# Optimization experiments

Measured on AMD Instinct MI355X. Metric: run time of the kernel, lower is better.

## Reference

```python
import jax, jax.numpy as jnp
import numpy as np

BITS = 8
EPS = 1e-08
D_IN = 4096
D_OUT = 4096


def setup_inputs() -> dict:
    key = jax.random.key(0)
    k1, k2, k3 = jax.random.split(key, 3)
    hidden_states = jax.random.normal(k1, (4, 2048, D_IN), dtype=jnp.float32)
    # Pre-quantized (dequantized-value) weight buffer, as the module stores it in float
    qmax = 2 ** (BITS - 1) - 1
    w = jax.random.normal(k2, (D_IN, D_OUT), dtype=jnp.float32) * 0.02
    w_scale = jnp.max(jnp.abs(w)) / qmax
    weight_quantized = jnp.clip(jnp.round(w / w_scale), -qmax, qmax) * w_scale
    bias = jax.random.normal(k3, (D_OUT,), dtype=jnp.float32) * 0.01
    x_scale = jnp.asarray(3.0, dtype=jnp.float32)  # calibrated activation maxabs
    return {
        "hidden_states": hidden_states,
        "weight_quantized": weight_quantized,
        "x_scale": x_scale,
        "bias": bias,
    }


def _quantize_maxabs(x, scale, bits, eps):
    # scalar max-abs quantization with a fixed (calibrated) scale
    qmax = 2 ** (bits - 1) - 1
    step = jnp.maximum(scale, eps) / qmax
    return jnp.clip(jnp.round(x / step), -qmax, qmax) * step


def reference(hidden_states, weight_quantized, x_scale, bias):
    orig_shape = hidden_states.shape[:-1]
    d = hidden_states.shape[-1]
    x_flat = hidden_states.reshape(-1, d)
    x_q = _quantize_maxabs(x_flat, x_scale, BITS, EPS).astype(weight_quantized.dtype)
    out = x_q @ weight_quantized  # [tokens, d_out]
    out = out + bias.astype(out.dtype)[None, :]
    out = out.astype(hidden_states.dtype)
    return out.reshape(*orig_shape, weight_quantized.shape[1])
```

## Files before the change

kernel.cpp:

```cpp
#include <hip/hip_runtime.h>
#include <hip/hip_bf16.h>
#include <cstdint>

#define D_IN  4096
#define D_OUT 4096

typedef __attribute__((ext_vector_type(4)))  int   i32x4;

typedef const __attribute__((address_space(1))) unsigned g_u32;
typedef __attribute__((address_space(3))) unsigned       l_u32;

__global__ void prep_kernel(const float* __restrict__ W, int nw,
                            const float* __restrict__ x,
                            char* __restrict__ xq,
                            const float* __restrict__ xscale, int nx,
                            unsigned* __restrict__ wsp) {
    int tid = threadIdx.x;
    if (blockIdx.x < 1024) {
        __shared__ float red[256];
        float m = 0.f;
        for (int i = (blockIdx.x * 256 + tid) * 4; i < nw; i += 1024 * 256 * 4) {
            float4 v = *(const float4*)(W + i);
            m = fmaxf(m, fmaxf(fmaxf(fabsf(v.x), fabsf(v.y)),
                               fmaxf(fabsf(v.z), fabsf(v.w))));
        }
        red[tid] = m; __syncthreads();
        for (int s = 128; s > 0; s >>= 1) {
            if (tid < s) red[tid] = fmaxf(red[tid], red[tid + s]);
            __syncthreads();
        }
        if (tid == 0) atomicMax(wsp, __float_as_uint(red[0]));
    } else {
        int i = ((blockIdx.x - 1024) * 256 + tid) * 4;
        if (i >= nx) return;
        float inv = 127.0f / fmaxf(xscale[0], 1e-8f);
        float4 v = *(const float4*)(x + i);
        char4 o;
        o.x = (char)fminf(fmaxf(rintf(v.x * inv), -127.f), 127.f);
        o.y = (char)fminf(fmaxf(rintf(v.y * inv), -127.f), 127.f);
        o.z = (char)fminf(fmaxf(rintf(v.z * inv), -127.f), 127.f);
        o.w = (char)fminf(fmaxf(rintf(v.w * inv), -127.f), 127.f);
        *(char4*)(xq + i) = o;
    }
}

__global__ void convW_kernel(const float* __restrict__ W,
                             char* __restrict__ Wt,
                             const unsigned* __restrict__ wsp) {
    __shared__ float tile[64][65];
    const float wmax = __uint_as_float(wsp[0]);
    const float inv  = 127.0f / wmax;
    const int n0 = blockIdx.x * 64, k0 = blockIdx.y * 64;
    const int t = threadIdx.x;
    {
        const int r = t >> 2, c0 = (t & 3) * 16;
        const float* src = W + (size_t)(k0 + r) * D_OUT + n0 + c0;
#pragma unroll
        for (int j = 0; j < 4; ++j) {
            float4 v = *(const float4*)(src + j * 4);
            tile[r][c0 + j * 4 + 0] = v.x;
            tile[r][c0 + j * 4 + 1] = v.y;
            tile[r][c0 + j * 4 + 2] = v.z;
            tile[r][c0 + j * 4 + 3] = v.w;
        }
    }
    __syncthreads();
    {
        const int n = t >> 2, kc = (t & 3) * 16;
        int4 pk;
        int* pw = (int*)&pk;
#pragma unroll
        for (int w = 0; w < 4; ++w) {
            unsigned word = 0;
#pragma unroll
            for (int j = 0; j < 4; ++j) {
                int q = (int)rintf(tile[kc + w * 4 + j][n] * inv);
                word |= ((unsigned)(unsigned char)(char)q) << (8 * j);
            }
            pw[w] = (int)word;
        }
        *(int4*)(Wt + (size_t)(n0 + n) * D_IN + k0 + kc) = pk;
    }
}

__global__ __launch_bounds__(512, 4)
void gemm_kernel(const char* __restrict__ A,
                 const char* __restrict__ Bt,
                 const float* __restrict__ bias,
                 const float* __restrict__ xscale,
                 const unsigned* __restrict__ wsp,
                 float* __restrict__ C, int M) {
    constexpr int K = D_IN, N = D_OUT;
    constexpr int NT = K / 64;
    __shared__ char lds[2 * 24576];

    const int tid  = threadIdx.x;
    const int lane = tid & 63;
    const int wid  = tid >> 6;
    const int wr   = wid >> 1;
    const int wc   = wid & 1;

    const int nTn = N / 128;
    const int nwg = gridDim.x;
    int bid = blockIdx.x;
    int q8 = nwg >> 3, r8 = nwg & 7;
    int xcd = bid & 7, idx = bid >> 3;
    int swz = (xcd < r8 ? xcd * (q8 + 1) : r8 * (q8 + 1) + (xcd - r8) * q8) + idx;
    const int tm = swz / nTn, tn = swz % nTn;
    const int row0 = tm * 256, col0 = tn * 128;

    int srcA0, srcA1, srcB0;
    {
        int p0 = tid * 16;
        int p1 = (512 + tid) * 16;
        int s0 = p0 ^ (((p0 >> 7) & 3) << 4);
        int s1 = p1 ^ (((p1 >> 7) & 3) << 4);
        srcA0 = (s0 >> 6) * K + (s0 & 63);
        srcA1 = (s1 >> 6) * K + (s1 & 63);
        srcB0 = srcA0;
    }
    const int dstA0 = tid * 16, dstA1 = (512 + tid) * 16, dstB0 = 16384 + tid * 16;

    const char* srcA = A  + (size_t)row0 * K;
    const char* srcB = Bt + (size_t)col0 * K;
    char* b0 = lds;
    char* b1 = lds + 24576;

    auto STAGE = [&](int t, char* buf) {
        __builtin_amdgcn_global_load_lds((g_u32*)(srcA + t * 64 + srcA0),
                                         (l_u32*)(buf + dstA0), 16, 0, 0);
        __builtin_amdgcn_global_load_lds((g_u32*)(srcA + t * 64 + srcA1),
                                         (l_u32*)(buf + dstA1), 16, 0, 0);
        __builtin_amdgcn_global_load_lds((g_u32*)(srcB + t * 64 + srcB0),
                                         (l_u32*)(buf + dstB0), 16, 0, 0);
    };

    STAGE(0, b0);
    STAGE(1, b1);

    i32x4 acc[4][4];
#pragma unroll
    for (int m = 0; m < 4; ++m)
#pragma unroll
        for (int n = 0; n < 4; ++n) acc[m][n] = (i32x4){0, 0, 0, 0};

    const int cOff  = (((lane >> 4) ^ ((lane >> 1) & 3)) << 4);
    const int aBase = (wr * 64 + (lane & 15)) * 64 + cOff;
    const int bBase = 16384 + (wc * 64 + (lane & 15)) * 64 + cOff;

    asm volatile("s_waitcnt vmcnt(3)" ::: "memory");

    auto KTILE = [&](int t, char* cur) {
        i32x4 a[4], b[4];
        __builtin_amdgcn_s_barrier();
#pragma unroll
        for (int n = 0; n < 4; ++n) b[n] = *(const i32x4*)(cur + bBase + n * 1024);
#pragma unroll
        for (int m = 0; m < 4; ++m) a[m] = *(const i32x4*)(cur + aBase + m * 1024);
        __builtin_amdgcn_s_setprio(1);
#pragma unroll
        for (int m = 0; m < 4; ++m)
#pragma unroll
            for (int n = 0; n < 4; ++n)
                acc[m][n] = __builtin_amdgcn_mfma_i32_16x16x64_i8(a[m], b[n], acc[m][n], 0, 0, 0);
        __builtin_amdgcn_s_setprio(0);

        __builtin_amdgcn_s_barrier();
        if (t + 2 < NT) {
            STAGE(t + 2, cur);
            asm volatile("s_waitcnt vmcnt(3)" ::: "memory");
        } else {
            asm volatile("s_waitcnt vmcnt(0)" ::: "memory");
        }
    };

    for (int t = 0; t < NT; t += 2) {
        KTILE(t,     b0);
        KTILE(t + 1, b1);
    }

    const float wmax  = __uint_as_float(wsp[0]);
    const float scale = (fmaxf(xscale[0], 1e-8f) * (1.0f / 127.0f)) * (wmax * (1.0f / 127.0f));
    const int lr = (lane >> 4) * 4, lc = lane & 15;
#pragma unroll
    for (int n = 0; n < 4; ++n) {
        int col = col0 + wc * 64 + n * 16 + lc;
        float bv = bias[col];
#pragma unroll
        for (int m = 0; m < 4; ++m) {
            int rowb = row0 + wr * 64 + m * 16 + lr;
            i32x4 v = acc[m][n];
#pragma unroll
            for (int r2 = 0; r2 < 4; ++r2)
                C[(size_t)(rowb + r2) * N + col] = (float)v[r2] * scale + bv;
        }
    }
}

extern "C" void kernel_launch(void* const* d_in, const int* in_sizes, int n_in,
                              void* d_out, int out_size, void* d_ws, size_t ws_size,
                              hipStream_t stream) {
    const float* x      = (const float*)d_in[0];
    const float* W      = (const float*)d_in[1];
    const float* xscale = (const float*)d_in[2];
    const float* bias   = (const float*)d_in[3];
    float* out = (float*)d_out;

    const int nx = in_sizes[0];
    const int nw = in_sizes[1];
    const int M  = nx / D_IN;

    char*     xq  = (char*)d_ws;
    char*     Wt  = (char*)d_ws + (size_t)nx;
    unsigned* wsp = (unsigned*)((char*)d_ws + (size_t)nx + nw);

    hipMemsetAsync(wsp, 0, 4, stream);

    int qblocks = nx / 4 / 256;
    prep_kernel<<<1024 + qblocks, 256, 0, stream>>>(W, nw, x, xq, xscale, nx, wsp);

    dim3 tb(256);
    dim3 tg(D_OUT / 64, D_IN / 64);
    convW_kernel<<<tg, tb, 0, stream>>>(W, Wt, wsp);

    int grid = (M / 256) * (D_OUT / 128);
    gemm_kernel<<<grid, 512, 0, stream>>>(xq, Wt, bias, xscale, wsp, out, M);
}
```

Measured before the change: 218.9 us.

## Load A tiles directly into registers and double K tile to 128

The int8 GEMM now stages only the B tile through LDS and loads A fragments straight from global memory into registers. A is software-pipelined one K-step ahead in ping-pong register arrays. The K tile doubles to 128 with an 8-way XOR swizzle, and launch bounds drop from 4 to 2 blocks per CU to make room for the extra registers. This cuts LDS traffic and footprint for A and halves the number of barriers. The cost is duplicated global reads of A across the two column waves, strided global access, higher register use and lower occupancy.

```diff
diff --git a/kernel.cpp b/kernel.cpp
--- a/kernel.cpp
+++ b/kernel.cpp
@@ -83,7 +83,7 @@
     }
 }
 
-__global__ __launch_bounds__(512, 4)
+__global__ __launch_bounds__(512, 2)
 void gemm_kernel(const char* __restrict__ A,
                  const char* __restrict__ Bt,
                  const float* __restrict__ bias,
@@ -91,8 +91,8 @@
                  const unsigned* __restrict__ wsp,
                  float* __restrict__ C, int M) {
     constexpr int K = D_IN, N = D_OUT;
-    constexpr int NT = K / 64;
-    __shared__ char lds[2 * 24576];
+    constexpr int NT = K / 128;
+    __shared__ char lds[2 * 16384];
 
     const int tid  = threadIdx.x;
     const int lane = tid & 63;
@@ -109,34 +109,40 @@
     const int tm = swz / nTn, tn = swz % nTn;
     const int row0 = tm * 256, col0 = tn * 128;
 
-    int srcA0, srcA1, srcB0;
-    {
-        int p0 = tid * 16;
-        int p1 = (512 + tid) * 16;
-        int s0 = p0 ^ (((p0 >> 7) & 3) << 4);
-        int s1 = p1 ^ (((p1 >> 7) & 3) << 4);
-        srcA0 = (s0 >> 6) * K + (s0 & 63);
-        srcA1 = (s1 >> 6) * K + (s1 & 63);
-        srcB0 = srcA0;
-    }
-    const int dstA0 = tid * 16, dstA1 = (512 + tid) * 16, dstB0 = 16384 + tid * 16;
-
-    const char* srcA = A  + (size_t)row0 * K;
+    int srcOff[2], dstOff[2];
+#pragma unroll
+    for (int i = 0; i < 2; ++i) {
+        int p  = (i * 512 + tid) * 16;
+        int sw = p ^ (((p >> 7) & 7) << 4);
+        dstOff[i] = p;
+        srcOff[i] = (sw >> 7) * K + (sw & 127);
+    }
+
     const char* srcB = Bt + (size_t)col0 * K;
     char* b0 = lds;
-    char* b1 = lds + 24576;
-
-    auto STAGE = [&](int t, char* buf) {
-        __builtin_amdgcn_global_load_lds((g_u32*)(srcA + t * 64 + srcA0),
-                                         (l_u32*)(buf + dstA0), 16, 0, 0);
-        __builtin_amdgcn_global_load_lds((g_u32*)(srcA + t * 64 + srcA1),
-                                         (l_u32*)(buf + dstA1), 16, 0, 0);
-        __builtin_amdgcn_global_load_lds((g_u32*)(srcB + t * 64 + srcB0),
-                                         (l_u32*)(buf + dstB0), 16, 0, 0);
+    char* b1 = lds + 16384;
+
+    auto STAGEB = [&](int t, char* buf) {
+#pragma unroll
+        for (int i = 0; i < 2; ++i)
+            __builtin_amdgcn_global_load_lds((g_u32*)(srcB + t * 128 + srcOff[i]),
+                                             (l_u32*)(buf + dstOff[i]), 16, 0, 0);
     };
 
-    STAGE(0, b0);
-    STAGE(1, b1);
+    const char* aG = A + ((size_t)(row0 + wr * 64 + (lane & 15))) * K
+                       + ((lane >> 4) * 16);
+
+    auto LOADA = [&](int t, i32x4 (&dst)[4][2]) {
+#pragma unroll
+        for (int m = 0; m < 4; ++m)
+#pragma unroll
+            for (int ks = 0; ks < 2; ++ks)
+                dst[m][ks] = *(const i32x4*)(aG + (size_t)m * 16 * K + t * 128 + ks * 64);
+    };
+
+    const int cp0 = (((lane >> 4) ^ (lane & 7)) << 4);
+    const int cp1 = cp0 ^ 64;
+    const int bRow = (wc * 64 + (lane & 15)) * 128;
 
     i32x4 acc[4][4];
 #pragma unroll
@@ -144,39 +150,44 @@
 #pragma unroll
         for (int n = 0; n < 4; ++n) acc[m][n] = (i32x4){0, 0, 0, 0};
 
-    const int cOff  = (((lane >> 4) ^ ((lane >> 1) & 3)) << 4);
-    const int aBase = (wr * 64 + (lane & 15)) * 64 + cOff;
-    const int bBase = 16384 + (wc * 64 + (lane & 15)) * 64 + cOff;
-
-    asm volatile("s_waitcnt vmcnt(3)" ::: "memory");
-
-    auto KTILE = [&](int t, char* cur) {
-        i32x4 a[4], b[4];
+    i32x4 aP[4][2], aN[4][2];
+
+    STAGEB(0, b0);
+    LOADA(0, aP);
+    STAGEB(1, b1);
+
+    auto KT = [&](int t, char* cur, i32x4 (&aUse)[4][2], i32x4 (&aLoad)[4][2],
+                  bool last) {
         __builtin_amdgcn_s_barrier();
-#pragma unroll
-        for (int n = 0; n < 4; ++n) b[n] = *(const i32x4*)(cur + bBase + n * 1024);
-#pragma unroll
-        for (int m = 0; m < 4; ++m) a[m] = *(const i32x4*)(cur + aBase + m * 1024);
+        if (last) { asm volatile("s_waitcnt vmcnt(0)" ::: "memory"); }
+        else      { asm volatile("s_waitcnt vmcnt(2)" ::: "memory"); }
+
+        i32x4 b[4][2];
+#pragma unroll
+        for (int n = 0; n < 4; ++n) {
+            b[n][0] = *(const i32x4*)(cur + bRow + n * 2048 + cp0);
+            b[n][1] = *(const i32x4*)(cur + bRow + n * 2048 + cp1);
+        }
+        if (t + 1 < NT) LOADA(t + 1, aLoad);
+
+        asm volatile("s_waitcnt lgkmcnt(0)" ::: "memory");
         __builtin_amdgcn_s_setprio(1);
 #pragma unroll
         for (int m = 0; m < 4; ++m)
 #pragma unroll
-            for (int n = 0; n < 4; ++n)
-                acc[m][n] = __builtin_amdgcn_mfma_i32_16x16x64_i8(a[m], b[n], acc[m][n], 0, 0, 0);
+            for (int n = 0; n < 4; ++n) {
+                acc[m][n] = __builtin_amdgcn_mfma_i32_16x16x64_i8(aUse[m][0], b[n][0], acc[m][n], 0, 0, 0);
+                acc[m][n] = __builtin_amdgcn_mfma_i32_16x16x64_i8(aUse[m][1], b[n][1], acc[m][n], 0, 0, 0);
+            }
         __builtin_amdgcn_s_setprio(0);
 
         __builtin_amdgcn_s_barrier();
-        if (t + 2 < NT) {
-            STAGE(t + 2, cur);
-            asm volatile("s_waitcnt vmcnt(3)" ::: "memory");
-        } else {
-            asm volatile("s_waitcnt vmcnt(0)" ::: "memory");
-        }
+        if (t + 2 < NT) STAGEB(t + 2, cur);
     };
 
     for (int t = 0; t < NT; t += 2) {
-        KTILE(t,     b0);
-        KTILE(t + 1, b1);
+        KT(t,     b0, aP, aN, false);
+        KT(t + 1, b1, aN, aP, t + 1 == NT - 1);
     }
 
     const float wmax  = __uint_as_float(wsp[0]);
```

Result: slower. 371.5 us (+69.7%).
